# Performance work log

Measured on AMD Instinct MI355X. Metric: run time of the kernel, lower is better.

Reference implementation:

```python
import jax, jax.numpy as jnp
import numpy as np
import math

# SLAYER SRM-alpha neuron constants (theta=10, tauSr=tauRef=10, Ts=1, scaleRef=2)
THETA = 10.0
TAU = 10.0
A = math.exp(-1.0 / TAU)          # per-step decay of alpha kernel
B1 = math.e * A / TAU             # k[1] where k[t] = (t/tau)*exp(1 - t/tau), k[0]=0
REF_SCALE = 2.0 * THETA           # refractory kernel = -scaleRef*theta * alpha(t)
SG_ALPHA = 10.0                   # surrogate width = tauRho * theta


def psp(x):
    """Causal alpha-kernel (SRM) filter along last (time) axis.
    y[t] = sum_{tau<t} k[t-tau] x[tau], realized as 2nd-order IIR:
    y[t] = 2A y[t-1] - A^2 y[t-2] + B1 x[t-1].
    x: [..., T] -> [..., T]
    """
    xt = jnp.moveaxis(x, -1, 0)  # [T, ...]
    z = jnp.zeros_like(xt[0])

    def step(c, x_t):
        y1, y2, xp = c
        y = 2.0 * A * y1 - (A * A) * y2 + B1 * xp
        return (y, y1, x_t), y

    _, ys = jax.lax.scan(step, (z, z, z), xt)
    return jnp.moveaxis(ys, 0, -1)


def spike(u):
    """SLAYER spike generation with refractory feedback.
    At each step, membrane u is reduced by -2*theta*alpha-filtered past spikes,
    then thresholded at theta. u: [..., T] -> binary spikes [..., T].
    """
    ut = jnp.moveaxis(u, -1, 0)
    z = jnp.zeros_like(ut[0])

    def step(c, u_t):
        y1, y2, sp = c
        y = 2.0 * A * y1 - (A * A) * y2 + B1 * sp  # alpha response to past spikes
        s = (u_t - REF_SCALE * y >= THETA).astype(u_t.dtype)
        return (y, y1, s), s

    _, ss = jax.lax.scan(step, (z, z, z), ut)
    return jnp.moveaxis(ss, 0, -1)


def conv2d_t(x, w, pad):
    """Per-timestep 2D conv. x: [B,C,H,W,T], w: [O,I,kh,kw]."""
    B, C, H, W, T = x.shape
    xb = jnp.moveaxis(x, -1, 1).reshape(B * T, C, H, W)
    y = jax.lax.conv_general_dilated(
        xb, w, window_strides=(1, 1), padding=[(pad, pad), (pad, pad)],
        dimension_numbers=("NCHW", "OIHW", "NCHW"))
    O = w.shape[0]
    return jnp.moveaxis(y.reshape(B, T, O, H, W), 1, -1)


def pool2(x):
    """SLAYER sum-pool: fixed conv with all weights = 1.1*theta, stride 2."""
    y = jax.lax.reduce_window(x, 0.0, jax.lax.add,
                              (1, 1, 2, 2, 1), (1, 1, 2, 2, 1), "VALID")
    return y * (1.1 * THETA)


def dense_t(x, w):
    """x: [B,C,H,W,T] or [B,F,T]; w: [O,F]. Flattens (C,H,W) -> F."""
    B = x.shape[0]
    T = x.shape[-1]
    f = x.reshape(B, -1, T)
    return jnp.einsum("of,bft->bot", w, f)


def setup_inputs() -> dict:
    key = jax.random.key(0)
    ks = jax.random.split(key, 6)
    B, T = 4, 100
    s_in = (jax.random.uniform(ks[0], (B, 2, 128, 128, T)) < 0.05).astype(jnp.float32)

    def mkw(k, shape, ws):
        fan = float(np.prod(shape[1:]))
        return jax.random.normal(k, shape, jnp.float32) * (ws / math.sqrt(fan))

    w1 = mkw(ks[1], (32, 2, 5, 5), 10.0)      # SC1, weightScale=10
    w2 = mkw(ks[2], (64, 32, 3, 3), 20.0)     # SC2, weightScale=20
    w3 = mkw(ks[3], (128, 64, 3, 3), 20.0)    # SC3, weightScale=20
    wf4a = mkw(ks[4], (512, 128 * 8 * 8), 1.0)  # SF4a
    wf4b = mkw(ks[5], (11, 512), 1.0)           # SF4b
    return {"s_in": s_in, "w1": w1, "w2": w2, "w3": w3, "wf4a": wf4a, "wf4b": wf4b}


def reference(s_in, w1, w2, w3, wf4a, wf4b):
    x = spike(psp(pool2(s_in)))                 # SP0: [B,2,64,64,T]
    x = spike(psp(conv2d_t(x, w1, pad=2)))      # SC1: [B,32,64,64,T]
    x = spike(psp(pool2(x)))                    # SP1: [B,32,32,32,T]
    x = spike(psp(conv2d_t(x, w2, pad=1)))      # SC2: [B,64,32,32,T]
    x = spike(psp(pool2(x)))                    # SP2: [B,64,16,16,T]
    x = spike(psp(conv2d_t(x, w3, pad=1)))      # SC3: [B,128,16,16,T]
    x = spike(psp(pool2(x)))                    # SP3: [B,128,8,8,T]
    x = spike(psp(dense_t(x, wf4a)))            # SF4a: [B,512,T]
    # SD4 dropout: identity at inference
    x = spike(psp(dense_t(x, wf4b)))            # SF4b: [B,11,T]
    return x
```

## Files before the change

kernel.cpp:

```cpp
#include <hip/hip_runtime.h>

typedef unsigned long long ull;

__device__ constexpr float C1f = (float)1.80967483607191914632;
__device__ constexpr float C2f = (float)0.81873075307798185867;
__device__ constexpr float C3f = (float)0.24596031111569496638;

__device__ __forceinline__ float iir_spike_step(float acc, float& y1, float& y2, float& xp,
                                                float& r1, float& r2, float& sp) {
#pragma clang fp contract(off)
    float u = C1f * y1 - C2f * y2 + C3f * xp;
    float r = C1f * r1 - C2f * r2 + C3f * sp;
    float s = (u - 20.0f * r >= 10.0f) ? 1.0f : 0.0f;
    y2 = y1; y1 = u; xp = acc;
    r2 = r1; r1 = r; sp = s;
    return s;
}

__device__ __forceinline__ void sparse_acc64(float& acc, ull m,
                                             const float* __restrict__ base, int lane) {
    while (m) {
        ull m1 = m & (m - 1);
        ull m2 = m1 & (m1 - 1);
        ull m3 = m2 & (m2 - 1);
        if (m3) {
            int c0 = __builtin_ctzll(m);
            int c1 = __builtin_ctzll(m1);
            int c2 = __builtin_ctzll(m2);
            int c3 = __builtin_ctzll(m3);
            float w0 = base[c0 * 64 + lane];
            float w1 = base[c1 * 64 + lane];
            float w2 = base[c2 * 64 + lane];
            float w3 = base[c3 * 64 + lane];
            acc += w0; acc += w1; acc += w2; acc += w3;
            m = m3 & (m3 - 1);
        } else {
            acc += base[__builtin_ctzll(m) * 64 + lane];
            m = m1;
        }
    }
}

__global__ void k_sp0(const float* __restrict__ s_in, ull* __restrict__ s0m) {
    int wid = (blockIdx.x * 256 + threadIdx.x) >> 6;
    int lane = threadIdx.x & 63;
    int h = wid & 63;
    int c = (wid >> 6) & 1;
    int b = wid >> 7;
    const float* p00 = s_in + ((size_t)(((b * 2 + c) * 128 + 2 * h) * 128 + 2 * lane)) * 100;
    const float* p01 = p00 + 100;
    const float* p10 = p00 + 12800;
    const float* p11 = p10 + 100;
    float y1 = 0, y2 = 0, xp = 0, r1 = 0, r2 = 0, sp = 0;
    for (int t = 0; t < 100; ++t) {
        float cnt = (p00[t] > 0.5f) + (p01[t] > 0.5f) + (p10[t] > 0.5f) + (p11[t] > 0.5f);
        float s = iir_spike_step(11.0f * cnt, y1, y2, xp, r1, r2, sp);
        ull m = __ballot(s > 0.5f);
        if (lane == 0) s0m[((size_t)(t * 4 + b) * 2 + c) * 64 + h] = m;
    }
}

__global__ void k_sc1(const ull* __restrict__ s0m, const float* __restrict__ w1,
                      ull* __restrict__ s1m) {
    int hg = blockIdx.x & 15;
    int o  = (blockIdx.x >> 4) & 31;
    int b  = blockIdx.x >> 9;
    __shared__ float wsm[50];
    for (int i = threadIdx.x; i < 50; i += 256) wsm[i] = w1[o * 50 + i];
    __syncthreads();
    int h = hg * 4 + (threadIdx.x >> 6);
    int lane = threadIdx.x & 63;
    int sh = lane - 2;
    float y1 = 0, y2 = 0, xp = 0, r1 = 0, r2 = 0, sp = 0;
    for (int t = 0; t < 100; ++t) {
        float acc = 0.0f;
        const ull* rb = s0m + (size_t)(t * 4 + b) * 128;
#pragma unroll
        for (int c = 0; c < 2; ++c) {
#pragma unroll
            for (int kh = 0; kh < 5; ++kh) {
                int ih = h - 2 + kh;
                ull m = (ih >= 0 && ih < 64) ? rb[c * 64 + ih] : 0ULL;
                unsigned pat = (sh >= 0) ? ((unsigned)(m >> sh) & 31u)
                                         : (((unsigned)m << (-sh)) & 31u);
                while (pat) {
                    int j = __builtin_ctz(pat);
                    pat &= pat - 1;
                    acc += wsm[c * 25 + kh * 5 + j];
                }
            }
        }
        float s = iir_spike_step(acc, y1, y2, xp, r1, r2, sp);
        ull mm = __ballot(s > 0.5f);
        if (lane == 0) s1m[((size_t)(t * 4 + b) * 32 + o) * 64 + h] = mm;
    }
}

__global__ void k_sp1(const ull* __restrict__ s1m, unsigned* __restrict__ s2m) {
    int wid = (blockIdx.x * 256 + threadIdx.x) >> 6;
    int lane = threadIdx.x & 63;
    int wop = wid & 15;
    int ho = (wid >> 4) & 31;
    int b = wid >> 9;
    int c = lane & 31;
    int q = lane >> 5;
    int w = wop * 2 + q;
    float y1 = 0, y2 = 0, xp = 0, r1 = 0, r2 = 0, sp = 0;
    for (int t = 0; t < 100; ++t) {
        const ull* base = s1m + ((size_t)(t * 4 + b) * 32 + c) * 64 + 2 * ho;
        ull m0 = base[0], m1 = base[1];
        unsigned v0 = (unsigned)(m0 >> (2 * w)) & 3u;
        unsigned v1 = (unsigned)(m1 >> (2 * w)) & 3u;
        float cnt = (float)((v0 & 1) + (v0 >> 1) + (v1 & 1) + (v1 >> 1));
        float s = iir_spike_step(11.0f * cnt, y1, y2, xp, r1, r2, sp);
        ull mm = __ballot(s > 0.5f);
        if (lane == 0)  s2m[((size_t)(t * 4 + b) * 32 + ho) * 32 + wop * 2]     = (unsigned)mm;
        if (lane == 32) s2m[((size_t)(t * 4 + b) * 32 + ho) * 32 + wop * 2 + 1] = (unsigned)(mm >> 32);
    }
}

__global__ void k_wT(const float* __restrict__ w2, const float* __restrict__ w3,
                     float* __restrict__ w2T, float* __restrict__ w3T) {
    int i = blockIdx.x * 256 + threadIdx.x;
    if (i < 9 * 32 * 64) {
        int o = i & 63; int c = (i >> 6) & 31; int p = i >> 11;
        w2T[i] = w2[(o * 32 + c) * 9 + p];
    }
    if (i < 9 * 64 * 128) {
        int o = i & 127; int c = (i >> 7) & 63; int p = i >> 13;
        w3T[i] = w3[(o * 64 + c) * 9 + p];
    }
}

__global__ void k_wT4a(const float* __restrict__ w, float* __restrict__ wT) {
    __shared__ float tile[64][65];
    int ft = blockIdx.x & 127;
    int ot = blockIdx.x >> 7;
    int j = threadIdx.x & 63;
    int i0 = threadIdx.x >> 6;
    for (int i = i0; i < 64; i += 4)
        tile[i][j] = w[(size_t)(ot * 64 + i) * 8192 + ft * 64 + j];
    __syncthreads();
    for (int i = i0; i < 64; i += 4)
        wT[(size_t)(ft * 64 + i) * 512 + ot * 64 + j] = tile[j][i];
}

__global__ __launch_bounds__(1024) void k_sc2(const unsigned* __restrict__ s2m,
                                              const float* __restrict__ w2T,
                                              ull* __restrict__ sc2m) {
    extern __shared__ float wl[];
    for (int i = threadIdx.x; i < 9 * 32 * 64; i += 1024) wl[i] = w2T[i];
    __syncthreads();
    int task = blockIdx.x * 16 + (threadIdx.x >> 6);
    int pix = task & 1023;
    int b = task >> 10;
    int h = pix >> 5, w = pix & 31;
    int lane = threadIdx.x & 63;
    float y1 = 0, y2 = 0, xp = 0, r1 = 0, r2 = 0, sp = 0;
    for (int t = 0; t < 100; ++t) {
        const unsigned* mb = s2m + (size_t)(t * 4 + b) * 1024;
        float acc = 0.0f;
#pragma unroll
        for (int kh = 0; kh < 3; ++kh) {
            int ih = h - 1 + kh;
            if (ih < 0 || ih >= 32) continue;
#pragma unroll
            for (int kw = 0; kw < 3; ++kw) {
                int iw = w - 1 + kw;
                if (iw < 0 || iw >= 32) continue;
                unsigned m = __builtin_amdgcn_readfirstlane(mb[ih * 32 + iw]);
                sparse_acc64(acc, (ull)m, wl + (kh * 3 + kw) * 32 * 64, lane);
            }
        }
        float s = iir_spike_step(acc, y1, y2, xp, r1, r2, sp);
        ull mm = __ballot(s > 0.5f);
        if (lane == 0) sc2m[(size_t)(t * 4 + b) * 1024 + pix] = mm;
    }
}

__global__ void k_sp2(const ull* __restrict__ sc2m, ull* __restrict__ s3m) {
    int wid = (blockIdx.x * 256 + threadIdx.x) >> 6;
    int lane = threadIdx.x & 63;
    int wo = wid & 15;
    int ho = (wid >> 4) & 15;
    int b = wid >> 8;
    float y1 = 0, y2 = 0, xp = 0, r1 = 0, r2 = 0, sp = 0;
    for (int t = 0; t < 100; ++t) {
        const ull* mb = sc2m + (size_t)(t * 4 + b) * 1024 + (2 * ho) * 32 + 2 * wo;
        ull a0 = mb[0], a1 = mb[1], a2 = mb[32], a3 = mb[33];
        float cnt = (float)(((a0 >> lane) & 1) + ((a1 >> lane) & 1) +
                            ((a2 >> lane) & 1) + ((a3 >> lane) & 1));
        float s = iir_spike_step(11.0f * cnt, y1, y2, xp, r1, r2, sp);
        ull mm = __ballot(s > 0.5f);
        if (lane == 0) s3m[(size_t)(t * 4 + b) * 256 + ho * 16 + wo] = mm;
    }
}

__global__ __launch_bounds__(512) void k_sc3(const ull* __restrict__ s3m,
                                             const float* __restrict__ w3T,
                                             ull* __restrict__ s4m) {
    extern __shared__ float wl[];
    int half = blockIdx.x & 1;
    int rest = blockIdx.x >> 1;
    int pg = rest & 31;
    int b = rest >> 5;
    for (int i = threadIdx.x; i < 9 * 64 * 64; i += 512) {
        int o = i & 63; int pc = i >> 6;
        wl[i] = w3T[pc * 128 + half * 64 + o];
    }
    __syncthreads();
    int pix = pg * 8 + (threadIdx.x >> 6);
    int h = pix >> 4, w = pix & 15;
    int lane = threadIdx.x & 63;
    float y1 = 0, y2 = 0, xp = 0, r1 = 0, r2 = 0, sp = 0;
    for (int t = 0; t < 100; ++t) {
        const ull* mb = s3m + (size_t)(t * 4 + b) * 256;
        float acc = 0.0f;
#pragma unroll
        for (int kh = 0; kh < 3; ++kh) {
            int ih = h - 1 + kh;
            if (ih < 0 || ih >= 16) continue;
#pragma unroll
            for (int kw = 0; kw < 3; ++kw) {
                int iw = w - 1 + kw;
                if (iw < 0 || iw >= 16) continue;
                ull mm64 = mb[ih * 16 + iw];
                unsigned lo = __builtin_amdgcn_readfirstlane((unsigned)mm64);
                unsigned hi = __builtin_amdgcn_readfirstlane((unsigned)(mm64 >> 32));
                ull m = ((ull)hi << 32) | lo;
                sparse_acc64(acc, m, wl + (kh * 3 + kw) * 64 * 64, lane);
            }
        }
        float s = iir_spike_step(acc, y1, y2, xp, r1, r2, sp);
        ull mm = __ballot(s > 0.5f);
        if (lane == 0) s4m[((size_t)(t * 4 + b) * 256 + pix) * 2 + half] = mm;
    }
}

__global__ void k_sp3(const ull* __restrict__ s4m, ull* __restrict__ s5m) {
    int wid = (blockIdx.x * 256 + threadIdx.x) >> 6;
    int lane = threadIdx.x & 63;
    int c = wid & 127;
    int b = wid >> 7;
    int half = c >> 6;
    int cbit = c & 63;
    int ho = lane >> 3, wo = lane & 7;
    float y1 = 0, y2 = 0, xp = 0, r1 = 0, r2 = 0, sp = 0;
    for (int t = 0; t < 100; ++t) {
        const ull* mb = s4m + ((size_t)(t * 4 + b) * 256 + (2 * ho) * 16 + 2 * wo) * 2 + half;
        ull a0 = mb[0], a1 = mb[2], a2 = mb[32], a3 = mb[34];
        float cnt = (float)(((a0 >> cbit) & 1) + ((a1 >> cbit) & 1) +
                            ((a2 >> cbit) & 1) + ((a3 >> cbit) & 1));
        float s = iir_spike_step(11.0f * cnt, y1, y2, xp, r1, r2, sp);
        ull mm = __ballot(s > 0.5f);
        if (lane == 0) s5m[(size_t)(t * 4 + b) * 128 + c] = mm;
    }
}

__global__ void k_gemm4a(const ull* __restrict__ s5m,
                         const float* __restrict__ wT,
                         float* __restrict__ acc_out) {
    int wg = blockIdx.x * 4 + (threadIdx.x >> 6);
    int lane = threadIdx.x & 63;
    int ot = wg & 7;
    int tb = wg >> 3;
    const ull* mp = s5m + (size_t)tb * 128;
    const float* wbase = wT + ot * 64 + lane;
    float acc = 0.0f;
    for (int c = 0; c < 128; ++c) {
        ull mv = mp[c];
        unsigned lo = __builtin_amdgcn_readfirstlane((unsigned)mv);
        unsigned hi = __builtin_amdgcn_readfirstlane((unsigned)(mv >> 32));
        ull m = ((ull)hi << 32) | lo;
        const float* wb = wbase + (size_t)(c * 64) * 512;
        while (m) {
            ull m1 = m & (m - 1);
            ull m2 = m1 & (m1 - 1);
            ull m3 = m2 & (m2 - 1);
            if (m3) {
                int c0 = __builtin_ctzll(m);
                int c1 = __builtin_ctzll(m1);
                int c2 = __builtin_ctzll(m2);
                int c3 = __builtin_ctzll(m3);
                float w0 = wb[(size_t)c0 * 512];
                float w1 = wb[(size_t)c1 * 512];
                float w2 = wb[(size_t)c2 * 512];
                float w3 = wb[(size_t)c3 * 512];
                acc += w0; acc += w1; acc += w2; acc += w3;
                m = m3 & (m3 - 1);
            } else {
                acc += wb[(size_t)__builtin_ctzll(m) * 512];
                m = m1;
            }
        }
    }
    acc_out[(size_t)tb * 512 + ot * 64 + lane] = acc;
}

__global__ void k_iir4a(const float* __restrict__ accbuf, unsigned char* __restrict__ s6) {
    int id = blockIdx.x * 64 + threadIdx.x;
    int b = id >> 9, o = id & 511;
    float y1 = 0, y2 = 0, xp = 0, r1 = 0, r2 = 0, sp = 0;
    for (int t = 0; t < 100; ++t) {
        float a = accbuf[(size_t)(t * 4 + b) * 512 + o];
        float s = iir_spike_step(a, y1, y2, xp, r1, r2, sp);
        s6[(size_t)(t * 4 + b) * 512 + o] = (unsigned char)s;
    }
}

__global__ void k_dense4b(const unsigned char* __restrict__ in,
                          const float* __restrict__ wt,
                          float* __restrict__ out) {
    int wid = blockIdx.x;
    int lane = threadIdx.x;
    int o = wid % 11;
    int b = wid / 11;
    float wreg[8];
    const float* wp = wt + o * 512 + lane * 8;
#pragma unroll
    for (int k = 0; k < 8; ++k) wreg[k] = wp[k];
    float y1 = 0, y2 = 0, xp = 0, r1 = 0, r2 = 0, sp = 0;
    for (int t = 0; t < 100; ++t) {
        const unsigned char* ip = in + (size_t)(t * 4 + b) * 512 + lane * 8;
        uchar4 a = *(const uchar4*)ip;
        uchar4 c = *(const uchar4*)(ip + 4);
        float acc = wreg[0] * (float)a.x + wreg[1] * (float)a.y +
                    wreg[2] * (float)a.z + wreg[3] * (float)a.w +
                    wreg[4] * (float)c.x + wreg[5] * (float)c.y +
                    wreg[6] * (float)c.z + wreg[7] * (float)c.w;
#pragma unroll
        for (int off = 32; off > 0; off >>= 1) acc += __shfl_xor(acc, off, 64);
        float s = iir_spike_step(acc, y1, y2, xp, r1, r2, sp);
        if (lane == 0) out[(b * 11 + o) * 100 + t] = s;
    }
}

extern "C" void kernel_launch(void* const* d_in, const int* in_sizes, int n_in,
                              void* d_out, int out_size, void* d_ws, size_t ws_size,
                              hipStream_t stream) {
    const float* s_in = (const float*)d_in[0];
    const float* w1   = (const float*)d_in[1];
    const float* w2   = (const float*)d_in[2];
    const float* w3   = (const float*)d_in[3];
    const float* w4a  = (const float*)d_in[4];
    const float* w4b  = (const float*)d_in[5];
    float* out = (float*)d_out;

    char* ws = (char*)d_ws;
    ull*           s0m  = (ull*)(ws + 0);
    ull*           s1m  = (ull*)(ws + 409600);
    unsigned*      s2m  = (unsigned*)(ws + 6963200);
    ull*           sc2m = (ull*)(ws + 8601600);
    ull*           s3m  = (ull*)(ws + 11878400);
    ull*           s4m  = (ull*)(ws + 12697600);
    ull*           s5m  = (ull*)(ws + 14336000);
    unsigned char* s6   = (unsigned char*)(ws + 14745600);
    float*         accA = (float*)(ws + 14950400);
    float*         w2T  = (float*)(ws + 15769600);
    float*         w3T  = (float*)(ws + 15843328);
    float*         wT4a = (float*)(ws + 16138240);

    hipFuncSetAttribute((const void*)k_sc2, hipFuncAttributeMaxDynamicSharedMemorySize, 73728);
    hipFuncSetAttribute((const void*)k_sc3, hipFuncAttributeMaxDynamicSharedMemorySize, 147456);

    k_wT<<<288, 256, 0, stream>>>(w2, w3, w2T, w3T);
    k_wT4a<<<1024, 256, 0, stream>>>(w4a, wT4a);
    k_sp0<<<128, 256, 0, stream>>>(s_in, s0m);
    k_sc1<<<2048, 256, 0, stream>>>(s0m, w1, s1m);
    k_sp1<<<512, 256, 0, stream>>>(s1m, s2m);
    k_sc2<<<256, 1024, 73728, stream>>>(s2m, w2T, sc2m);
    k_sp2<<<256, 256, 0, stream>>>(sc2m, s3m);
    k_sc3<<<256, 512, 147456, stream>>>(s3m, w3T, s4m);
    k_sp3<<<128, 256, 0, stream>>>(s4m, s5m);
    k_gemm4a<<<800, 256, 0, stream>>>(s5m, wT4a, accA);
    k_iir4a<<<32, 64, 0, stream>>>(accA, s6);
    k_dense4b<<<44, 64, 0, stream>>>(s6, w4b, out);
}
```

Baseline: 1.517 ms.

## Split conv weights between LDS and global, register-cache SC1 weights branchlessly

SC2 and SC3 now keep only the first four kernel positions' weights in static shared memory and read the other five directly from global memory, which cuts LDS use per block so more blocks can be resident. SC1 loads its 50 weights into registers and replaces the data-dependent ctz loop with a fixed 5-tap masked FMA loop to avoid divergence. The sparse accumulate helper becomes a stride template that the dense layer reuses. The cost is more global/L2 weight traffic in the conv layers and higher register pressure in SC1. The FMA rewrite also changes the floating-point summation order.

```diff
diff --git a/kernel.cpp b/kernel.cpp
--- a/kernel.cpp
+++ b/kernel.cpp
@@ -17,8 +17,8 @@
     return s;
 }
 
-__device__ __forceinline__ void sparse_acc64(float& acc, ull m,
-                                             const float* __restrict__ base, int lane) {
+template <int STRIDE>
+__device__ __forceinline__ void sacc(float& acc, ull m, const float* __restrict__ ptr) {
     while (m) {
         ull m1 = m & (m - 1);
         ull m2 = m1 & (m1 - 1);
@@ -28,14 +28,14 @@
             int c1 = __builtin_ctzll(m1);
             int c2 = __builtin_ctzll(m2);
             int c3 = __builtin_ctzll(m3);
-            float w0 = base[c0 * 64 + lane];
-            float w1 = base[c1 * 64 + lane];
-            float w2 = base[c2 * 64 + lane];
-            float w3 = base[c3 * 64 + lane];
+            float w0 = ptr[c0 * STRIDE];
+            float w1 = ptr[c1 * STRIDE];
+            float w2 = ptr[c2 * STRIDE];
+            float w3 = ptr[c3 * STRIDE];
             acc += w0; acc += w1; acc += w2; acc += w3;
             m = m3 & (m3 - 1);
         } else {
-            acc += base[__builtin_ctzll(m) * 64 + lane];
+            acc += ptr[__builtin_ctzll(m) * STRIDE];
             m = m1;
         }
     }
@@ -65,9 +65,9 @@
     int hg = blockIdx.x & 15;
     int o  = (blockIdx.x >> 4) & 31;
     int b  = blockIdx.x >> 9;
-    __shared__ float wsm[50];
-    for (int i = threadIdx.x; i < 50; i += 256) wsm[i] = w1[o * 50 + i];
-    __syncthreads();
+    float wr[50];
+#pragma unroll
+    for (int i = 0; i < 50; ++i) wr[i] = w1[o * 50 + i];
     int h = hg * 4 + (threadIdx.x >> 6);
     int lane = threadIdx.x & 63;
     int sh = lane - 2;
@@ -83,11 +83,9 @@
                 ull m = (ih >= 0 && ih < 64) ? rb[c * 64 + ih] : 0ULL;
                 unsigned pat = (sh >= 0) ? ((unsigned)(m >> sh) & 31u)
                                          : (((unsigned)m << (-sh)) & 31u);
-                while (pat) {
-                    int j = __builtin_ctz(pat);
-                    pat &= pat - 1;
-                    acc += wsm[c * 25 + kh * 5 + j];
-                }
+#pragma unroll
+                for (int j = 0; j < 5; ++j)
+                    acc = fmaf((float)((pat >> j) & 1u), wr[c * 25 + kh * 5 + j], acc);
             }
         }
         float s = iir_spike_step(acc, y1, y2, xp, r1, r2, sp);
@@ -148,8 +146,8 @@
 __global__ __launch_bounds__(1024) void k_sc2(const unsigned* __restrict__ s2m,
                                               const float* __restrict__ w2T,
                                               ull* __restrict__ sc2m) {
-    extern __shared__ float wl[];
-    for (int i = threadIdx.x; i < 9 * 32 * 64; i += 1024) wl[i] = w2T[i];
+    __shared__ float wl[4 * 32 * 64];
+    for (int i = threadIdx.x; i < 4 * 32 * 64; i += 1024) wl[i] = w2T[i];
     __syncthreads();
     int task = blockIdx.x * 16 + (threadIdx.x >> 6);
     int pix = task & 1023;
@@ -169,7 +167,9 @@
                 int iw = w - 1 + kw;
                 if (iw < 0 || iw >= 32) continue;
                 unsigned m = __builtin_amdgcn_readfirstlane(mb[ih * 32 + iw]);
-                sparse_acc64(acc, (ull)m, wl + (kh * 3 + kw) * 32 * 64, lane);
+                int pos = kh * 3 + kw;
+                if (pos < 4) sacc<64>(acc, (ull)m, wl  + pos * 2048 + lane);
+                else         sacc<64>(acc, (ull)m, w2T + pos * 2048 + lane);
             }
         }
         float s = iir_spike_step(acc, y1, y2, xp, r1, r2, sp);
@@ -199,12 +199,12 @@
 __global__ __launch_bounds__(512) void k_sc3(const ull* __restrict__ s3m,
                                              const float* __restrict__ w3T,
                                              ull* __restrict__ s4m) {
-    extern __shared__ float wl[];
+    __shared__ float wl[4 * 64 * 64];
     int half = blockIdx.x & 1;
     int rest = blockIdx.x >> 1;
     int pg = rest & 31;
     int b = rest >> 5;
-    for (int i = threadIdx.x; i < 9 * 64 * 64; i += 512) {
+    for (int i = threadIdx.x; i < 4 * 64 * 64; i += 512) {
         int o = i & 63; int pc = i >> 6;
         wl[i] = w3T[pc * 128 + half * 64 + o];
     }
@@ -212,6 +212,7 @@
     int pix = pg * 8 + (threadIdx.x >> 6);
     int h = pix >> 4, w = pix & 15;
     int lane = threadIdx.x & 63;
+    const float* wg = w3T + half * 64 + lane;
     float y1 = 0, y2 = 0, xp = 0, r1 = 0, r2 = 0, sp = 0;
     for (int t = 0; t < 100; ++t) {
         const ull* mb = s3m + (size_t)(t * 4 + b) * 256;
@@ -228,7 +229,9 @@
                 unsigned lo = __builtin_amdgcn_readfirstlane((unsigned)mm64);
                 unsigned hi = __builtin_amdgcn_readfirstlane((unsigned)(mm64 >> 32));
                 ull m = ((ull)hi << 32) | lo;
-                sparse_acc64(acc, m, wl + (kh * 3 + kw) * 64 * 64, lane);
+                int pos = kh * 3 + kw;
+                if (pos < 4) sacc<64>(acc, m, wl + pos * 4096 + lane);
+                else         sacc<128>(acc, m, wg + pos * 64 * 128);
             }
         }
         float s = iir_spike_step(acc, y1, y2, xp, r1, r2, sp);
@@ -272,27 +275,7 @@
         unsigned lo = __builtin_amdgcn_readfirstlane((unsigned)mv);
         unsigned hi = __builtin_amdgcn_readfirstlane((unsigned)(mv >> 32));
         ull m = ((ull)hi << 32) | lo;
-        const float* wb = wbase + (size_t)(c * 64) * 512;
-        while (m) {
-            ull m1 = m & (m - 1);
-            ull m2 = m1 & (m1 - 1);
-            ull m3 = m2 & (m2 - 1);
-            if (m3) {
-                int c0 = __builtin_ctzll(m);
-                int c1 = __builtin_ctzll(m1);
-                int c2 = __builtin_ctzll(m2);
-                int c3 = __builtin_ctzll(m3);
-                float w0 = wb[(size_t)c0 * 512];
-                float w1 = wb[(size_t)c1 * 512];
-                float w2 = wb[(size_t)c2 * 512];
-                float w3 = wb[(size_t)c3 * 512];
-                acc += w0; acc += w1; acc += w2; acc += w3;
-                m = m3 & (m3 - 1);
-            } else {
-                acc += wb[(size_t)__builtin_ctzll(m) * 512];
-                m = m1;
-            }
-        }
+        sacc<512>(acc, m, wbase + (size_t)(c * 64) * 512);
     }
     acc_out[(size_t)tb * 512 + ot * 64 + lane] = acc;
 }
@@ -360,17 +343,14 @@
     float*         w3T  = (float*)(ws + 15843328);
     float*         wT4a = (float*)(ws + 16138240);
 
-    hipFuncSetAttribute((const void*)k_sc2, hipFuncAttributeMaxDynamicSharedMemorySize, 73728);
-    hipFuncSetAttribute((const void*)k_sc3, hipFuncAttributeMaxDynamicSharedMemorySize, 147456);
-
     k_wT<<<288, 256, 0, stream>>>(w2, w3, w2T, w3T);
     k_wT4a<<<1024, 256, 0, stream>>>(w4a, wT4a);
     k_sp0<<<128, 256, 0, stream>>>(s_in, s0m);
     k_sc1<<<2048, 256, 0, stream>>>(s0m, w1, s1m);
     k_sp1<<<512, 256, 0, stream>>>(s1m, s2m);
-    k_sc2<<<256, 1024, 73728, stream>>>(s2m, w2T, sc2m);
+    k_sc2<<<256, 1024, 0, stream>>>(s2m, w2T, sc2m);
     k_sp2<<<256, 256, 0, stream>>>(sc2m, s3m);
-    k_sc3<<<256, 512, 147456, stream>>>(s3m, w3T, s4m);
+    k_sc3<<<256, 512, 0, stream>>>(s3m, w3T, s4m);
     k_sp3<<<128, 256, 0, stream>>>(s4m, s5m);
     k_gemm4a<<<800, 256, 0, stream>>>(s5m, wT4a, accA);
     k_iir4a<<<32, 64, 0, stream>>>(accA, s6);
```

Measured after the change: 1.581 ms. +4.2%, slower.
